# Performance work log

Hardware: AMD Instinct MI355X
Metric: run time of the kernel (lower is better)

Reference implementation:

```python
import jax, jax.numpy as jnp
import numpy as np

DT = 0.03
SEQ_LEN = 30
STEER_RATE = 0.4
B = 2097152


def clip_by_tensor(t, t_min, t_max):
    # Faithful to original: (t>min)*t + (t<min)*min, then (r<=max)*r + (r>max)*max.
    # Note: when t == t_min the result is 0, matching the torch code's quirk.
    r = (t > t_min).astype(t.dtype) * t + (t < t_min).astype(t.dtype) * t_min
    r = (r <= t_max).astype(r.dtype) * r + (r > t_max).astype(r.dtype) * t_max
    return r


def setup_inputs() -> dict:
    key = jax.random.key(0)
    k1, k2 = jax.random.split(key)
    z = jax.random.normal(k1, (B, 2), dtype=jnp.float32)
    init_state = jax.random.normal(k2, (B, 6), dtype=jnp.float32)
    return {"z": z, "init_state": init_state}


def reference(z, init_state):
    last_st = init_state[:, 5]
    state0 = init_state[:, :4]  # [B,4] = x, y, psi, v

    steering = z[:, 1] * 0.5
    d_steer = STEER_RATE * DT
    steering = clip_by_tensor(steering, last_st - d_steer, last_st + d_steer)
    steering = jnp.clip(steering, -0.5, 0.5)
    pedal = z[:, 0] * 2.5

    # controls are constant across steps; clamps are idempotent
    beta = jnp.clip(steering, -0.5, 0.5)
    a_t = jnp.clip(pedal, -2.5, 2.5)
    tan_beta = jnp.tan(beta)

    def step(state, _):
        x_t, y_t, psi_t, v_t = state[:, 0], state[:, 1], state[:, 2], state[:, 3]
        v_t1 = jnp.clip(v_t + a_t * DT, 0.0, 10.0)
        psi_t1 = (v_t * tan_beta / 2.5) * DT + psi_t
        x_t1 = v_t1 * jnp.cos(psi_t1) * DT + x_t
        y_t1 = v_t1 * jnp.sin(psi_t1) * DT + y_t
        new_state = jnp.stack([x_t1, y_t1, psi_t1, v_t1], axis=1)
        return new_state, new_state

    _, traj = jax.lax.scan(step, state0, None, length=SEQ_LEN)  # [T,B,4]
    return jnp.transpose(traj, (1, 0, 2))  # [B,T,4]
```

## Files before the change

kernel.cpp:

```cpp
#include <hip/hip_runtime.h>

#define DT 0.03f
#define SEQ_LEN 30
#define D_STEER (0.4f * 0.03f)

#define BT 64
#define PAD 31

typedef float f32x2 __attribute__((ext_vector_type(2)));
typedef float f32x4 __attribute__((ext_vector_type(4)));

__global__ __launch_bounds__(64) void ccdec_kernel(
    const float* __restrict__ z,
    const float* __restrict__ init_state,
    float* __restrict__ out,
    int B, int ntiles, int grid)
{
    __shared__ f32x4 lds[BT * PAD];

    const int tid = threadIdx.x;

    int t0 = (int)(((long long)blockIdx.x       * ntiles) / grid);
    int t1 = (int)(((long long)(blockIdx.x + 1) * ntiles) / grid);

    for (int tile = t0; tile < t1; ++tile) {
        int b  = tile * BT + tid;
        bool valid = (b < B);
        int bb = valid ? b : (B - 1);

        f32x2 zv  = *(reinterpret_cast<const f32x2*>(z) + (size_t)bb);
        const f32x2* stp = reinterpret_cast<const f32x2*>(init_state) + 3ull * (size_t)bb;
        f32x2 s01 = stp[0];
        f32x2 s23 = stp[1];
        f32x2 s45 = stp[2];

        float x   = s01.x;
        float y   = s01.y;
        float psi = s23.x;
        float v   = s23.y;
        float last_st = s45.y;

        float steering = zv.y * 0.5f;
        float tmin = last_st - D_STEER;
        float tmax = last_st + D_STEER;
        float r = (steering > tmin) ? steering : ((steering < tmin) ? tmin : 0.0f);
        r = (r <= tmax) ? r : tmax;
        steering = fminf(fmaxf(r, -0.5f), 0.5f);

        float pedal = zv.x * 2.5f;
        float beta  = fminf(fmaxf(steering, -0.5f), 0.5f);
        float a_t   = fminf(fmaxf(pedal, -2.5f), 2.5f);
        float tan_beta = __tanf(beta);
        float dpsi_k   = tan_beta * (1.0f / 2.5f) * DT;
        float adt      = a_t * DT;

        bool full_tile = ((tile + 1) * BT <= B);

        if (full_tile) {
            #pragma unroll
            for (int t = 0; t < SEQ_LEN; ++t) {
                float v1 = fminf(fmaxf(v + adt, 0.0f), 10.0f);
                psi = v * dpsi_k + psi;
                float s, c;
                __sincosf(psi, &s, &c);
                x = v1 * c * DT + x;
                y = v1 * s * DT + y;
                v = v1;
                f32x4 o; o.x = x; o.y = y; o.z = psi; o.w = v;
                lds[tid * PAD + t] = o;
            }
            __syncthreads();

            f32x4* outp4 = reinterpret_cast<f32x4*>(out) + (size_t)tile * BT * SEQ_LEN;
            #pragma unroll
            for (int m = 0; m < SEQ_LEN; ++m) {
                int f  = tid + m * BT;
                int rr = f / SEQ_LEN;
                int jj = f - rr * SEQ_LEN;
                outp4[f] = lds[rr * PAD + jj];
            }
        } else {
            if (valid) {
                f32x4* outp = reinterpret_cast<f32x4*>(out) + (size_t)b * SEQ_LEN;
                #pragma unroll
                for (int t = 0; t < SEQ_LEN; ++t) {
                    float v1 = fminf(fmaxf(v + adt, 0.0f), 10.0f);
                    psi = v * dpsi_k + psi;
                    float s, c;
                    __sincosf(psi, &s, &c);
                    x = v1 * c * DT + x;
                    y = v1 * s * DT + y;
                    v = v1;
                    f32x4 o; o.x = x; o.y = y; o.z = psi; o.w = v;
                    outp[t] = o;
                }
            }
        }
        __syncthreads();
    }
}

extern "C" void kernel_launch(void* const* d_in, const int* in_sizes, int n_in,
                              void* d_out, int out_size, void* d_ws, size_t ws_size,
                              hipStream_t stream)
{
    const float* z          = (const float*)d_in[0];
    const float* init_state = (const float*)d_in[1];
    float* out = (float*)d_out;

    int B = in_sizes[0] / 2;
    int ntiles = (B + BT - 1) / BT;
    int grid = 256 * 5;
    if (grid > ntiles) grid = ntiles;
    ccdec_kernel<<<grid, BT, 0, stream>>>(z, init_state, out, B, ntiles, grid);
}
```

Measured before the change: 223.1 us.

## Prefetch next tile inputs during output store and drop block barriers

Loads the next tile's z and init_state values into registers while the current tile's trajectory is being copied from LDS to global memory, so input load latency overlaps the store phase. Also removes the __syncthreads calls, relying on the block being a single 64-lane wavefront so LDS writes and reads stay ordered within the wave. This adds a few live registers and depends on the one-wave-per-block assumption for correctness.

```diff
diff --git a/kernel.cpp b/kernel.cpp
--- a/kernel.cpp
+++ b/kernel.cpp
@@ -22,18 +22,17 @@
 
     int t0 = (int)(((long long)blockIdx.x       * ntiles) / grid);
     int t1 = (int)(((long long)(blockIdx.x + 1) * ntiles) / grid);
+    if (t0 >= t1) return;
+
+    int b0  = t0 * BT + tid;
+    int bb0 = (b0 < B) ? b0 : (B - 1);
+    f32x2 zv  = *(reinterpret_cast<const f32x2*>(z) + (size_t)bb0);
+    const f32x2* stp0 = reinterpret_cast<const f32x2*>(init_state) + 3ull * (size_t)bb0;
+    f32x2 s01 = stp0[0];
+    f32x2 s23 = stp0[1];
+    f32x2 s45 = stp0[2];
 
     for (int tile = t0; tile < t1; ++tile) {
-        int b  = tile * BT + tid;
-        bool valid = (b < B);
-        int bb = valid ? b : (B - 1);
-
-        f32x2 zv  = *(reinterpret_cast<const f32x2*>(z) + (size_t)bb);
-        const f32x2* stp = reinterpret_cast<const f32x2*>(init_state) + 3ull * (size_t)bb;
-        f32x2 s01 = stp[0];
-        f32x2 s23 = stp[1];
-        f32x2 s45 = stp[2];
-
         float x   = s01.x;
         float y   = s01.y;
         float psi = s23.x;
@@ -69,7 +68,16 @@
                 f32x4 o; o.x = x; o.y = y; o.z = psi; o.w = v;
                 lds[tid * PAD + t] = o;
             }
-            __syncthreads();
+
+            if (tile + 1 < t1) {
+                int nb  = (tile + 1) * BT + tid;
+                int nbb = (nb < B) ? nb : (B - 1);
+                zv  = *(reinterpret_cast<const f32x2*>(z) + (size_t)nbb);
+                const f32x2* nstp = reinterpret_cast<const f32x2*>(init_state) + 3ull * (size_t)nbb;
+                s01 = nstp[0];
+                s23 = nstp[1];
+                s45 = nstp[2];
+            }
 
             f32x4* outp4 = reinterpret_cast<f32x4*>(out) + (size_t)tile * BT * SEQ_LEN;
             #pragma unroll
@@ -80,8 +88,9 @@
                 outp4[f] = lds[rr * PAD + jj];
             }
         } else {
-            if (valid) {
-                f32x4* outp = reinterpret_cast<f32x4*>(out) + (size_t)b * SEQ_LEN;
+            int wb = tile * BT + tid;
+            if (wb < B) {
+                f32x4* outp = reinterpret_cast<f32x4*>(out) + (size_t)wb * SEQ_LEN;
                 #pragma unroll
                 for (int t = 0; t < SEQ_LEN; ++t) {
                     float v1 = fminf(fmaxf(v + adt, 0.0f), 10.0f);
@@ -95,8 +104,16 @@
                     outp[t] = o;
                 }
             }
+            if (tile + 1 < t1) {
+                int nb  = (tile + 1) * BT + tid;
+                int nbb = (nb < B) ? nb : (B - 1);
+                zv  = *(reinterpret_cast<const f32x2*>(z) + (size_t)nbb);
+                const f32x2* nstp = reinterpret_cast<const f32x2*>(init_state) + 3ull * (size_t)nbb;
+                s01 = nstp[0];
+                s23 = nstp[1];
+                s45 = nstp[2];
+            }
         }
-        __syncthreads();
     }
 }
 
```

Result: slower. 231.8 us (+3.9%).

## Launch one 128-thread block per tile with redundant compute and split stores

Applied to the files above, without the earlier changes.

Replaces the persistent grid-stride loop over 64-row tiles with one block per tile, launched at 128 threads. Both waves redundantly simulate the same 64 rows and each fills the whole LDS staging buffer, so every wave reads back only what it wrote itself and the __syncthreads barriers can go. The coalesced output copy is then split across the two waves, each doing half of it. The cost is twice the trajectory arithmetic and duplicate LDS writes, in exchange for more in-flight memory traffic and no barriers. The kernel is already close to store-bandwidth bound.

```diff
diff --git a/kernel.cpp b/kernel.cpp
--- a/kernel.cpp
+++ b/kernel.cpp
@@ -4,59 +4,82 @@
 #define SEQ_LEN 30
 #define D_STEER (0.4f * 0.03f)
 
-#define BT 64
-#define PAD 31
+#define ROWS 64
+#define NT   128
+#define PAD  31
 
 typedef float f32x2 __attribute__((ext_vector_type(2)));
 typedef float f32x4 __attribute__((ext_vector_type(4)));
 
-__global__ __launch_bounds__(64) void ccdec_kernel(
+__global__ __launch_bounds__(NT) void ccdec_kernel(
     const float* __restrict__ z,
     const float* __restrict__ init_state,
     float* __restrict__ out,
-    int B, int ntiles, int grid)
+    int B)
 {
-    __shared__ f32x4 lds[BT * PAD];
+    __shared__ f32x4 lds[ROWS * PAD];
 
-    const int tid = threadIdx.x;
+    const int tid  = threadIdx.x;
+    const int lane = tid & 63;
+    const int tile = blockIdx.x;
 
-    int t0 = (int)(((long long)blockIdx.x       * ntiles) / grid);
-    int t1 = (int)(((long long)(blockIdx.x + 1) * ntiles) / grid);
+    int b  = tile * ROWS + lane;
+    bool valid = (b < B);
+    int bb = valid ? b : (B - 1);
 
-    for (int tile = t0; tile < t1; ++tile) {
-        int b  = tile * BT + tid;
-        bool valid = (b < B);
-        int bb = valid ? b : (B - 1);
+    f32x2 zv  = *(reinterpret_cast<const f32x2*>(z) + (size_t)bb);
+    const f32x2* stp = reinterpret_cast<const f32x2*>(init_state) + 3ull * (size_t)bb;
+    f32x2 s01 = stp[0];
+    f32x2 s23 = stp[1];
+    f32x2 s45 = stp[2];
 
-        f32x2 zv  = *(reinterpret_cast<const f32x2*>(z) + (size_t)bb);
-        const f32x2* stp = reinterpret_cast<const f32x2*>(init_state) + 3ull * (size_t)bb;
-        f32x2 s01 = stp[0];
-        f32x2 s23 = stp[1];
-        f32x2 s45 = stp[2];
+    float x   = s01.x;
+    float y   = s01.y;
+    float psi = s23.x;
+    float v   = s23.y;
+    float last_st = s45.y;
 
-        float x   = s01.x;
-        float y   = s01.y;
-        float psi = s23.x;
-        float v   = s23.y;
-        float last_st = s45.y;
+    float steering = zv.y * 0.5f;
+    float tmin = last_st - D_STEER;
+    float tmax = last_st + D_STEER;
+    float r = (steering > tmin) ? steering : ((steering < tmin) ? tmin : 0.0f);
+    r = (r <= tmax) ? r : tmax;
+    steering = fminf(fmaxf(r, -0.5f), 0.5f);
 
-        float steering = zv.y * 0.5f;
-        float tmin = last_st - D_STEER;
-        float tmax = last_st + D_STEER;
-        float r = (steering > tmin) ? steering : ((steering < tmin) ? tmin : 0.0f);
-        r = (r <= tmax) ? r : tmax;
-        steering = fminf(fmaxf(r, -0.5f), 0.5f);
+    float pedal = zv.x * 2.5f;
+    float beta  = fminf(fmaxf(steering, -0.5f), 0.5f);
+    float a_t   = fminf(fmaxf(pedal, -2.5f), 2.5f);
+    float tan_beta = __tanf(beta);
+    float dpsi_k   = tan_beta * (1.0f / 2.5f) * DT;
+    float adt      = a_t * DT;
 
-        float pedal = zv.x * 2.5f;
-        float beta  = fminf(fmaxf(steering, -0.5f), 0.5f);
-        float a_t   = fminf(fmaxf(pedal, -2.5f), 2.5f);
-        float tan_beta = __tanf(beta);
-        float dpsi_k   = tan_beta * (1.0f / 2.5f) * DT;
-        float adt      = a_t * DT;
+    bool full_tile = ((tile + 1) * ROWS <= B);
 
-        bool full_tile = ((tile + 1) * BT <= B);
+    if (full_tile) {
+        #pragma unroll
+        for (int t = 0; t < SEQ_LEN; ++t) {
+            float v1 = fminf(fmaxf(v + adt, 0.0f), 10.0f);
+            psi = v * dpsi_k + psi;
+            float s, c;
+            __sincosf(psi, &s, &c);
+            x = v1 * c * DT + x;
+            y = v1 * s * DT + y;
+            v = v1;
+            f32x4 o; o.x = x; o.y = y; o.z = psi; o.w = v;
+            lds[lane * PAD + t] = o;
+        }
 
-        if (full_tile) {
+        f32x4* outp4 = reinterpret_cast<f32x4*>(out) + (size_t)tile * ROWS * SEQ_LEN;
+        #pragma unroll
+        for (int m = 0; m < SEQ_LEN / 2; ++m) {
+            int f  = tid + m * NT;
+            int rr = f / SEQ_LEN;
+            int jj = f - rr * SEQ_LEN;
+            outp4[f] = lds[rr * PAD + jj];
+        }
+    } else {
+        if (valid && tid < 64) {
+            f32x4* outp = reinterpret_cast<f32x4*>(out) + (size_t)b * SEQ_LEN;
             #pragma unroll
             for (int t = 0; t < SEQ_LEN; ++t) {
                 float v1 = fminf(fmaxf(v + adt, 0.0f), 10.0f);
@@ -67,36 +90,9 @@
                 y = v1 * s * DT + y;
                 v = v1;
                 f32x4 o; o.x = x; o.y = y; o.z = psi; o.w = v;
-                lds[tid * PAD + t] = o;
-            }
-            __syncthreads();
-
-            f32x4* outp4 = reinterpret_cast<f32x4*>(out) + (size_t)tile * BT * SEQ_LEN;
-            #pragma unroll
-            for (int m = 0; m < SEQ_LEN; ++m) {
-                int f  = tid + m * BT;
-                int rr = f / SEQ_LEN;
-                int jj = f - rr * SEQ_LEN;
-                outp4[f] = lds[rr * PAD + jj];
-            }
-        } else {
-            if (valid) {
-                f32x4* outp = reinterpret_cast<f32x4*>(out) + (size_t)b * SEQ_LEN;
-                #pragma unroll
-                for (int t = 0; t < SEQ_LEN; ++t) {
-                    float v1 = fminf(fmaxf(v + adt, 0.0f), 10.0f);
-                    psi = v * dpsi_k + psi;
-                    float s, c;
-                    __sincosf(psi, &s, &c);
-                    x = v1 * c * DT + x;
-                    y = v1 * s * DT + y;
-                    v = v1;
-                    f32x4 o; o.x = x; o.y = y; o.z = psi; o.w = v;
-                    outp[t] = o;
-                }
+                outp[t] = o;
             }
         }
-        __syncthreads();
     }
 }
 
@@ -109,8 +105,6 @@
     float* out = (float*)d_out;
 
     int B = in_sizes[0] / 2;
-    int ntiles = (B + BT - 1) / BT;
-    int grid = 256 * 5;
-    if (grid > ntiles) grid = ntiles;
-    ccdec_kernel<<<grid, BT, 0, stream>>>(z, init_state, out, B, ntiles, grid);
+    int ntiles = (B + ROWS - 1) / ROWS;
+    ccdec_kernel<<<ntiles, NT, 0, stream>>>(z, init_state, out, B);
 }
```

New measurement: 187.6 us. 15.9% less time.
